# Kernel optimization log

Hardware: AMD Instinct MI355X
Metric: run time of the kernel (lower is better)

The kernel has to match this reference:

```python
import jax, jax.numpy as jnp
import numpy as np

NUM_FREQS = 256
FRAME_SIZE = 5
LOOKAHEAD = 0

B, T, F_TOTAL = 8, 4096, 481


def setup_inputs() -> dict:
    key = jax.random.key(0)
    k1, k2 = jax.random.split(key)
    spec = jax.random.normal(k1, (B, 2, T, F_TOTAL), dtype=jnp.float32)
    coefs = jax.random.normal(k2, (B, 2 * FRAME_SIZE, T, NUM_FREQS), dtype=jnp.float32)
    return {"spec": spec, "coefs": coefs}


def reference(spec, coefs):
    # spec:  [B, 2, T, F_total]  (real/imag channels)
    # coefs: [B, 2*frame_size, T, num_freqs]
    Bc, _, Tc, Fq = coefs.shape
    df = spec[..., :NUM_FREQS]  # [B, 2, T, Fq]
    # causal pad along time: (frame_size-1-lookahead) before, lookahead after
    padded = jnp.pad(df, ((0, 0), (0, 0), (FRAME_SIZE - 1 - LOOKAHEAD, LOOKAHEAD), (0, 0)))
    # unfold over time -> [B, 2, T, Fq, frame_size]
    frames = jnp.stack([padded[:, :, k:k + Tc, :] for k in range(FRAME_SIZE)], axis=-1)
    # coefs -> [B, 2, T, Fq, frame_size]
    c = coefs.reshape(Bc, 2, FRAME_SIZE, Tc, Fq).transpose(0, 1, 3, 4, 2)
    pr, pi = frames[:, 0], frames[:, 1]
    cr, ci = c[:, 0], c[:, 1]
    real = jnp.sum(pr * cr - pi * ci, axis=-1)  # [B, T, Fq]
    imag = jnp.sum(pi * cr + pr * ci, axis=-1)
    spec_f = jnp.stack([real, imag], axis=1)    # [B, 2, T, Fq]
    return jnp.concatenate([spec_f, spec[..., NUM_FREQS:]], axis=-1)
```

## Files before the change

kernel.cpp:

```cpp
#include <hip/hip_runtime.h>


static constexpr int kB  = 8;
static constexpr int kT  = 4096;
static constexpr int kFT = 481;
static constexpr int kNF = 256;
static constexpr int kFS = 5;

__global__ __launch_bounds__(256) void df_filter(const float* __restrict__ spec,
                                                 const float* __restrict__ coefs,
                                                 float* __restrict__ out) {
    int idx = blockIdx.x * 256 + threadIdx.x;
    int f4 = idx & 63;
    int b  = (idx >> 6) & 7;
    int t  = idx >> 9;
    int f  = f4 << 2;

    const float* cr_base = coefs + ((size_t)(b * 10    ) * kT + t) * kNF + f;
    const float* ci_base = coefs + ((size_t)(b * 10 + 5) * kT + t) * kNF + f;
    const float* sr_base = spec + ((size_t)(b * 2    ) * kT) * kFT + f;
    const float* si_base = spec + ((size_t)(b * 2 + 1) * kT) * kFT + f;

    float accR[4] = {0.f, 0.f, 0.f, 0.f};
    float accI[4] = {0.f, 0.f, 0.f, 0.f};

#pragma unroll
    for (int k = 0; k < kFS; ++k) {
        int tk = t + k - (kFS - 1);
        if (tk >= 0) {
            float4 cr = *(const float4*)(cr_base + (size_t)k * kT * kNF);
            float4 ci = *(const float4*)(ci_base + (size_t)k * kT * kNF);
            const float* pr = sr_base + (size_t)tk * kFT;
            const float* pi = si_base + (size_t)tk * kFT;
            float crv[4] = {cr.x, cr.y, cr.z, cr.w};
            float civ[4] = {ci.x, ci.y, ci.z, ci.w};
#pragma unroll
            for (int j = 0; j < 4; ++j) {
                float prv = pr[j];
                float piv = pi[j];
                accR[j] = fmaf(prv, crv[j], fmaf(-piv, civ[j], accR[j]));
                accI[j] = fmaf(piv, crv[j], fmaf( prv, civ[j], accI[j]));
            }
        }
    }

    float* outR = out + ((size_t)(b * 2    ) * kT + t) * kFT + f;
    float* outI = out + ((size_t)(b * 2 + 1) * kT + t) * kFT + f;
#pragma unroll
    for (int j = 0; j < 4; ++j) {
        outR[j] = accR[j];
        outI[j] = accI[j];
    }
}

__global__ __launch_bounds__(256) void df_tail(const float* __restrict__ spec,
                                               float* __restrict__ out) {
    int row = blockIdx.x;
    int f   = threadIdx.x;
    if (f < kFT - kNF) {
        size_t off = (size_t)row * kFT + kNF + f;
        out[off] = spec[off];
    }
}

extern "C" void kernel_launch(void* const* d_in, const int* in_sizes, int n_in,
                              void* d_out, int out_size, void* d_ws, size_t ws_size,
                              hipStream_t stream) {
    const float* spec  = (const float*)d_in[0];
    const float* coefs = (const float*)d_in[1];
    float* out = (float*)d_out;

    df_filter<<<(kB * kT * (kNF / 4)) / 256, 256, 0, stream>>>(spec, coefs, out);
    df_tail<<<kB * 2 * kT, 256, 0, stream>>>(spec, out);
}
```

Measured before the change: 580.0 us.

## Fuse tail copy into filter kernel and register-tile spec window over time

Merges the two launches into one kernel: each thread now handles four consecutive time steps, keeps a sliding window of spec values in registers so overlapping frames reuse loads, and then runs a grid-stride loop that copies the untouched tail frequencies. Coefficient loads and output stores are marked nontemporal so the streamed data does not pollute the cache. The aim is to cut the extra launch and the repeated spec reads. The cost is fewer threads, higher register use per thread, and a tail copy that uses integer division per element.

Measured after the change: 567.2 us. 1.02x faster.

```diff
diff --git a/kernel.cpp b/kernel.cpp
--- a/kernel.cpp
+++ b/kernel.cpp
@@ -6,60 +6,75 @@
 static constexpr int kFT = 481;
 static constexpr int kNF = 256;
 static constexpr int kFS = 5;
+static constexpr int kTT = 4;
+static constexpr int kWin = kTT + kFS - 1;
+static constexpr int kTailF = kFT - kNF;
+static constexpr unsigned kTailElems = (unsigned)kB * 2u * kT * kTailF;
 
-__global__ __launch_bounds__(256) void df_filter(const float* __restrict__ spec,
-                                                 const float* __restrict__ coefs,
-                                                 float* __restrict__ out) {
-    int idx = blockIdx.x * 256 + threadIdx.x;
-    int f4 = idx & 63;
-    int b  = (idx >> 6) & 7;
-    int t  = idx >> 9;
-    int f  = f4 << 2;
+typedef float v4f __attribute__((ext_vector_type(4)));
 
-    const float* cr_base = coefs + ((size_t)(b * 10    ) * kT + t) * kNF + f;
-    const float* ci_base = coefs + ((size_t)(b * 10 + 5) * kT + t) * kNF + f;
-    const float* sr_base = spec + ((size_t)(b * 2    ) * kT) * kFT + f;
-    const float* si_base = spec + ((size_t)(b * 2 + 1) * kT) * kFT + f;
+__global__ __launch_bounds__(256) void df_fused(const float* __restrict__ spec,
+                                                const float* __restrict__ coefs,
+                                                float* __restrict__ out) {
+    const int idx = blockIdx.x * 256 + threadIdx.x;
+    const int f4 = idx & 63;
+    const int b  = (idx >> 6) & 7;
+    const int tg = idx >> 9;
+    const int t0 = tg * kTT;
+    const int f  = f4 << 2;
 
-    float accR[4] = {0.f, 0.f, 0.f, 0.f};
-    float accI[4] = {0.f, 0.f, 0.f, 0.f};
+    const float* sr = spec + (size_t)(b * 2    ) * kT * kFT + f;
+    const float* si = spec + (size_t)(b * 2 + 1) * kT * kFT + f;
 
+    float prw[kWin][4];
+    float piw[kWin][4];
 #pragma unroll
-    for (int k = 0; k < kFS; ++k) {
-        int tk = t + k - (kFS - 1);
+    for (int r = 0; r < kWin; ++r) {
+        const int tk = t0 - (kFS - 1) + r;
         if (tk >= 0) {
-            float4 cr = *(const float4*)(cr_base + (size_t)k * kT * kNF);
-            float4 ci = *(const float4*)(ci_base + (size_t)k * kT * kNF);
-            const float* pr = sr_base + (size_t)tk * kFT;
-            const float* pi = si_base + (size_t)tk * kFT;
-            float crv[4] = {cr.x, cr.y, cr.z, cr.w};
-            float civ[4] = {ci.x, ci.y, ci.z, ci.w};
+            const float* pr = sr + (size_t)tk * kFT;
+            const float* pi = si + (size_t)tk * kFT;
 #pragma unroll
-            for (int j = 0; j < 4; ++j) {
-                float prv = pr[j];
-                float piv = pi[j];
-                accR[j] = fmaf(prv, crv[j], fmaf(-piv, civ[j], accR[j]));
-                accI[j] = fmaf(piv, crv[j], fmaf( prv, civ[j], accI[j]));
-            }
+            for (int j = 0; j < 4; ++j) { prw[r][j] = pr[j]; piw[r][j] = pi[j]; }
+        } else {
+#pragma unroll
+            for (int j = 0; j < 4; ++j) { prw[r][j] = 0.f; piw[r][j] = 0.f; }
         }
     }
 
-    float* outR = out + ((size_t)(b * 2    ) * kT + t) * kFT + f;
-    float* outI = out + ((size_t)(b * 2 + 1) * kT + t) * kFT + f;
 #pragma unroll
-    for (int j = 0; j < 4; ++j) {
-        outR[j] = accR[j];
-        outI[j] = accI[j];
+    for (int tt = 0; tt < kTT; ++tt) {
+        const int t = t0 + tt;
+        float accR[4] = {0.f, 0.f, 0.f, 0.f};
+        float accI[4] = {0.f, 0.f, 0.f, 0.f};
+#pragma unroll
+        for (int k = 0; k < kFS; ++k) {
+            const v4f cr = __builtin_nontemporal_load(
+                (const v4f*)(coefs + ((size_t)(b * 10 + k    ) * kT + t) * kNF + f));
+            const v4f ci = __builtin_nontemporal_load(
+                (const v4f*)(coefs + ((size_t)(b * 10 + 5 + k) * kT + t) * kNF + f));
+            const int r = tt + k;
+#pragma unroll
+            for (int j = 0; j < 4; ++j) {
+                accR[j] = fmaf(prw[r][j], cr[j], fmaf(-piw[r][j], ci[j], accR[j]));
+                accI[j] = fmaf(piw[r][j], cr[j], fmaf( prw[r][j], ci[j], accI[j]));
+            }
+        }
+        float* oR = out + ((size_t)(b * 2    ) * kT + t) * kFT + f;
+        float* oI = out + ((size_t)(b * 2 + 1) * kT + t) * kFT + f;
+#pragma unroll
+        for (int j = 0; j < 4; ++j) {
+            __builtin_nontemporal_store(accR[j], oR + j);
+            __builtin_nontemporal_store(accI[j], oI + j);
+        }
     }
-}
 
-__global__ __launch_bounds__(256) void df_tail(const float* __restrict__ spec,
-                                               float* __restrict__ out) {
-    int row = blockIdx.x;
-    int f   = threadIdx.x;
-    if (f < kFT - kNF) {
-        size_t off = (size_t)row * kFT + kNF + f;
-        out[off] = spec[off];
+    const unsigned gsz = gridDim.x * 256u;
+    for (unsigned i = (unsigned)idx; i < kTailElems; i += gsz) {
+        const unsigned row = i / (unsigned)kTailF;
+        const unsigned col = i - row * (unsigned)kTailF;
+        const size_t off = (size_t)row * kFT + kNF + col;
+        __builtin_nontemporal_store(__builtin_nontemporal_load(spec + off), out + off);
     }
 }
 
@@ -70,6 +85,5 @@
     const float* coefs = (const float*)d_in[1];
     float* out = (float*)d_out;
 
-    df_filter<<<(kB * kT * (kNF / 4)) / 256, 256, 0, stream>>>(spec, coefs, out);
-    df_tail<<<kB * 2 * kT, 256, 0, stream>>>(spec, out);
+    df_fused<<<(kB * (kT / kTT) * (kNF / 4)) / 256, 256, 0, stream>>>(spec, coefs, out);
 }
```
